# Optimization experiments

Hardware: AMD Instinct MI355X
Metric: run time of the kernel (lower is better)

Reference implementation:

```python
import jax, jax.numpy as jnp
import numpy as np

W0 = 30.0  # Sine frequency


def _bilinear_sample(plane, gx, gy):
    """torch.grid_sample(mode='bilinear', padding_mode='zeros', align_corners=True).
    plane: (C,H,W); gx,gy: (P,) normalized coords in [-1,1]. Returns (P,C)."""
    C, H, W = plane.shape
    ix = (gx + 1.0) * 0.5 * (W - 1)
    iy = (gy + 1.0) * 0.5 * (H - 1)
    x0 = jnp.floor(ix); y0 = jnp.floor(iy)
    x1 = x0 + 1.0;      y1 = y0 + 1.0
    wx1 = ix - x0; wx0 = 1.0 - wx1
    wy1 = iy - y0; wy0 = 1.0 - wy1

    def corner(xc, yc, w):
        valid = ((xc >= 0) & (xc <= W - 1) & (yc >= 0) & (yc <= H - 1)).astype(plane.dtype)
        xi = jnp.clip(xc, 0, W - 1).astype(jnp.int32)
        yi = jnp.clip(yc, 0, H - 1).astype(jnp.int32)
        return plane[:, yi, xi] * (w * valid)  # (C,P)

    out = (corner(x0, y0, wx0 * wy0) + corner(x1, y0, wx1 * wy0)
           + corner(x0, y1, wx0 * wy1) + corner(x1, y1, wx1 * wy1))
    return out.T  # (P,C)


def setup_inputs() -> dict:
    key = jax.random.key(0)
    ks = jax.random.split(key, 8)
    N = 500_000
    C, H, W = 128, 256, 256
    coords = jax.random.uniform(ks[0], (1, N, 3), jnp.float32, minval=-1.0, maxval=1.0)
    planes = [jax.random.normal(ks[1 + i], (1, C, H, W), jnp.float32) * 0.1 for i in range(3)]
    # Linear weights: first layer sine init, then frequency_init(30) for layers 2,3
    W1 = jax.random.uniform(ks[4], (C, C), jnp.float32, minval=-1.0 / C, maxval=1.0 / C)
    lim = np.sqrt(6.0 / C) / W0
    W2 = jax.random.uniform(ks[5], (C, C), jnp.float32, minval=-lim, maxval=lim)
    W3 = jax.random.uniform(ks[6], (1, C), jnp.float32, minval=-lim, maxval=lim)
    return {
        "coordinates": coords,
        "plane_xy": planes[0], "plane_yz": planes[1], "plane_xz": planes[2],
        "W1": W1, "b1": jnp.zeros((C,), jnp.float32),
        "W2": W2, "b2": jnp.zeros((C,), jnp.float32),
        "W3": W3, "b3": jnp.zeros((1,), jnp.float32),
    }


def reference(coordinates, plane_xy, plane_yz, plane_xz, W1, b1, W2, b2, W3, b3):
    B, N, _ = coordinates.shape  # B must be 1 (plane batch is 1, as in torch)
    c = coordinates.reshape(-1, 3)
    p0 = plane_xy[0]
    # NOTE: original module samples the *xz* coords from embeddings[0] (plane_xy) —
    # a bug we faithfully preserve — and multiplies [xy, xz, xz]; yz_embed is unused.
    xy = _bilinear_sample(p0, c[:, 0], c[:, 1])  # (P,C)
    xz = _bilinear_sample(p0, c[:, 0], c[:, 2])  # (P,C)
    features = xy * xz * xz
    h = jnp.sin(W0 * (features @ W1.T + b1))
    h = jnp.sin(W0 * (h @ W2.T + b2))
    out = h @ W3.T + b3
    return out.reshape(B, N, 1)
```

## Files before the change

### kernel.cpp

```cpp
#include <hip/hip_runtime.h>
#include <hip/hip_fp16.h>

typedef float f32x4 __attribute__((ext_vector_type(4)));
typedef _Float16 f16x8 __attribute__((ext_vector_type(8)));

#define CDIM 128
#define HW 256
#define NBINS 256
#define BINCAP 2560
#define TILES_PER_BIN 10
#define BINS_PER_XCD 32
#define GRID_MAIN 256

#define LDS_FENCE() asm volatile("" ::: "memory")

__global__ __launch_bounds__(256) void k_transpose(const float* __restrict__ plane,
                                                   unsigned short* __restrict__ planeT) {
    __shared__ unsigned short tile[32][130];
    int tid = threadIdx.x;
    int y  = blockIdx.x >> 3;
    int x0 = (blockIdx.x & 7) * 32;
    int tx = tid & 31, tc = tid >> 5;
    for (int cc = 0; cc < 128; cc += 8) {
        int c = cc + tc;
        float v = plane[c * (HW * HW) + y * HW + x0 + tx];
        tile[tx][c] = __half_as_ushort(__float2half(v));
    }
    __syncthreads();
    for (int it = 0; it < 16; ++it) {
        int idx = it * 256 + tid;
        int c = idx & 127, xi = idx >> 7;
        planeT[(y * HW + x0 + xi) * CDIM + c] = tile[xi][c];
    }
}

__global__ __launch_bounds__(256) void k_wconv(const float* __restrict__ W1,
                                               const float* __restrict__ W2,
                                               unsigned short* __restrict__ W1h,
                                               unsigned short* __restrict__ W2h) {
    int i = blockIdx.x * 256 + threadIdx.x;
    if (i < 16384) W1h[i] = __half_as_ushort(__float2half(W1[i]));
    else           W2h[i - 16384] = __half_as_ushort(__float2half(W2[i - 16384]));
}

__global__ __launch_bounds__(256) void k_scatter(const float* __restrict__ coords,
                                                 float4* __restrict__ bins,
                                                 int* __restrict__ cursor, int N) {
    __shared__ int hist[NBINS];
    __shared__ int rnk[NBINS];
    __shared__ int base[NBINS];
    const int tid = threadIdx.x;
    hist[tid] = 0; rnk[tid] = 0;
    __syncthreads();

    const int start = blockIdx.x * 2048;
    float gx[8], gy[8], gz[8]; int bn[8];
#pragma unroll
    for (int k = 0; k < 8; ++k) {
        int p = start + k * 256 + tid;
        if (p < N) {
            gx[k] = coords[p * 3 + 0];
            gy[k] = coords[p * 3 + 1];
            gz[k] = coords[p * 3 + 2];
            float ix = (gx[k] + 1.f) * 127.5f;
            bn[k] = max(0, min((int)floorf(ix), HW - 1));
            atomicAdd(&hist[bn[k]], 1);
        } else bn[k] = -1;
    }
    __syncthreads();
    if (hist[tid] > 0) base[tid] = atomicAdd(&cursor[tid], hist[tid]);
    __syncthreads();
#pragma unroll
    for (int k = 0; k < 8; ++k) {
        if (bn[k] >= 0) {
            int p = start + k * 256 + tid;
            int r = atomicAdd(&rnk[bn[k]], 1);
            int pos = base[bn[k]] + r;
            if (pos < BINCAP) {
                float4 rec; rec.x = gx[k]; rec.y = gy[k]; rec.z = gz[k];
                rec.w = __int_as_float(p);
                bins[(size_t)bn[k] * BINCAP + pos] = rec;
            }
        }
    }
}

struct PrepT {
    int off[8];
    __half2 w[4];
    __half2 v[4];
};

__device__ __forceinline__ PrepT prepV(float gx, float gy, float gz, int cg) {
    PrepT r;
    float ix = (gx + 1.f) * 127.5f;
    float iy = (gy + 1.f) * 127.5f;
    float iz = (gz + 1.f) * 127.5f;
    float xf = floorf(ix), yf = floorf(iy), zf = floorf(iz);
    float wx1 = ix - xf, wy1 = iy - yf, wz1 = iz - zf;
    float wx0 = 1.f - wx1, wy0 = 1.f - wy1, wz0 = 1.f - wz1;
    int x0 = max(0, min((int)xf, HW - 1));
    int y0 = max(0, min((int)yf, HW - 1));
    int z0 = max(0, min((int)zf, HW - 1));
    int x1 = min(x0 + 1, HW - 1);
    int y1 = min(y0 + 1, HW - 1);
    int z1 = min(z0 + 1, HW - 1);
    int cx0 = x0 * CDIM + cg * 8, cx1 = x1 * CDIM + cg * 8;
    r.off[0] = (y0 << 15) + cx0; r.off[1] = (y0 << 15) + cx1;
    r.off[2] = (y1 << 15) + cx0; r.off[3] = (y1 << 15) + cx1;
    r.off[4] = (z0 << 15) + cx0; r.off[5] = (z0 << 15) + cx1;
    r.off[6] = (z1 << 15) + cx0; r.off[7] = (z1 << 15) + cx1;
    r.w[0] = __float2half2_rn(wy0 * wx0);
    r.w[1] = __float2half2_rn(wy0 * wx1);
    r.w[2] = __float2half2_rn(wy1 * wx0);
    r.w[3] = __float2half2_rn(wy1 * wx1);
    r.v[0] = __float2half2_rn(wz0 * wx0);
    r.v[1] = __float2half2_rn(wz0 * wx1);
    r.v[2] = __float2half2_rn(wz1 * wx0);
    r.v[3] = __float2half2_rn(wz1 * wx1);
    return r;
}

struct LdT { uint4 d[8]; };

__device__ __forceinline__ LdT ld8(const unsigned short* __restrict__ planeT, const PrepT& a) {
    LdT r;
#pragma unroll
    for (int c = 0; c < 8; ++c)
        r.d[c] = *reinterpret_cast<const uint4*>(planeT + a.off[c]);
    return r;
}

__device__ __forceinline__ __half2 geth2(const uint4& u, int g) {
    const unsigned* p = reinterpret_cast<const unsigned*>(&u);
    return __builtin_bit_cast(__half2, p[g]);
}

__device__ __forceinline__ void interp_store(unsigned short* dst, const PrepT& a, const LdT& L) {
    unsigned o[4];
#pragma unroll
    for (int g = 0; g < 4; ++g) {
        __half2 xy = __hmul2(a.w[0], geth2(L.d[0], g));
        xy = __hfma2(a.w[1], geth2(L.d[1], g), xy);
        xy = __hfma2(a.w[2], geth2(L.d[2], g), xy);
        xy = __hfma2(a.w[3], geth2(L.d[3], g), xy);
        __half2 xz = __hmul2(a.v[0], geth2(L.d[4], g));
        xz = __hfma2(a.v[1], geth2(L.d[5], g), xz);
        xz = __hfma2(a.v[2], geth2(L.d[6], g), xz);
        xz = __hfma2(a.v[3], geth2(L.d[7], g), xz);
        __half2 f = __hmul2(xy, __hmul2(xz, xz));
        o[g] = __builtin_bit_cast(unsigned, f);
    }
    uint4 pack; pack.x = o[0]; pack.y = o[1]; pack.z = o[2]; pack.w = o[3];
    *reinterpret_cast<uint4*>(dst) = pack;
}

template <bool SORTED>
__global__ __launch_bounds__(1024, 4) void k_all(const float* __restrict__ coords,
                                                 const float4* __restrict__ bins,
                                                 const int* __restrict__ cursor,
                                                 const unsigned short* __restrict__ planeT,
                                                 const unsigned short* __restrict__ W1h,
                                                 const unsigned short* __restrict__ W2h,
                                                 const float* __restrict__ b1,
                                                 const float* __restrict__ b2,
                                                 const float* __restrict__ W3,
                                                 const float* __restrict__ b3,
                                                 float* __restrict__ out, int N) {
    __shared__ alignas(16) uint4 W1L[128][16];
    __shared__ alignas(16) uint4 W2L[128][16];
    __shared__ alignas(16) unsigned short featS[256][128];

    const int tid  = threadIdx.x;
    const int wave = tid >> 6, lane = tid & 63;
    const int ro   = wave * 16;
    const int j = lane & 15, rg = lane >> 4;
    const int pt = lane >> 4, cg = lane & 15;

#pragma unroll
    for (int i = 0; i < 2; ++i) {
        int idx = i * 1024 + tid;
        int row = idx >> 4, col = idx & 15;
        W1L[row][col ^ (row & 15)] = reinterpret_cast<const uint4*>(W1h)[idx];
        W2L[row][col ^ (row & 15)] = reinterpret_cast<const uint4*>(W2h)[idx];
    }
    float b1v[8], b2v[8], w3v[8];
#pragma unroll
    for (int nt = 0; nt < 8; ++nt) {
        b1v[nt] = 30.f * b1[nt * 16 + j];
        b2v[nt] = 30.f * b2[nt * 16 + j];
        w3v[nt] = W3[nt * 16 + j];
    }
    const float bb3 = b3[0];
    __syncthreads();

    const int ntt = SORTED ? (NBINS * TILES_PER_BIN) : ((N + 255) >> 8);
    for (int tt = blockIdx.x; tt < ntt; tt += gridDim.x) {
        int bin = 0, base = 0, cnt = 0, pbase = 0;
        if (SORTED) {
            int xcd = tt & 7, jj = tt >> 3;
            bin  = xcd * BINS_PER_XCD + jj / TILES_PER_BIN;
            base = (jj % TILES_PER_BIN) * 256;
            cnt  = min(cursor[bin], BINCAP);
            if (base >= cnt) continue;
        } else {
            pbase = tt * 256 + ro;
        }
        const float4* brec = bins + (size_t)bin * BINCAP;

        {
            PrepT a0, a1, a2, a3;
#pragma unroll
            for (int it = 0; it < 4; ++it) {
                float gx, gy, gz;
                if (SORTED) {
                    int q = min(base + ro + it * 4 + pt, cnt - 1);
                    float4 s = brec[q];
                    gx = s.x; gy = s.y; gz = s.z;
                } else {
                    int p = min(pbase + it * 4 + pt, N - 1);
                    gx = coords[p * 3 + 0];
                    gy = coords[p * 3 + 1];
                    gz = coords[p * 3 + 2];
                }
                PrepT a = prepV(gx, gy, gz, cg);
                if (it == 0) a0 = a; else if (it == 1) a1 = a;
                else if (it == 2) a2 = a; else a3 = a;
            }
            LdT d0 = ld8(planeT, a0);
            LdT d1 = ld8(planeT, a1);
            LdT d2 = ld8(planeT, a2);
            LdT d3 = ld8(planeT, a3);
            interp_store(&featS[ro + 0 * 4 + pt][(cg ^ (0 * 4 + pt)) * 8], a0, d0);
            interp_store(&featS[ro + 1 * 4 + pt][(cg ^ (1 * 4 + pt)) * 8], a1, d1);
            interp_store(&featS[ro + 2 * 4 + pt][(cg ^ (2 * 4 + pt)) * 8], a2, d2);
            interp_store(&featS[ro + 3 * 4 + pt][(cg ^ (3 * 4 + pt)) * 8], a3, d3);
        }

        LDS_FENCE();

        f32x4 acc[8];
#pragma unroll
        for (int nt = 0; nt < 8; ++nt) acc[nt] = (f32x4){0.f, 0.f, 0.f, 0.f};

        f16x8 af[4];
#pragma unroll
        for (int kk = 0; kk < 4; ++kk)
            af[kk] = __builtin_bit_cast(f16x8, *reinterpret_cast<const uint4*>(&featS[ro + j][((kk * 4 + rg) ^ j) * 8]));

#pragma unroll
        for (int kk = 0; kk < 4; ++kk) {
            f16x8 bf[8];
#pragma unroll
            for (int nt = 0; nt < 8; ++nt)
                bf[nt] = __builtin_bit_cast(f16x8, W1L[nt * 16 + j][(kk * 4 + rg) ^ j]);
#pragma unroll
            for (int nt = 0; nt < 8; ++nt)
                acc[nt] = __builtin_amdgcn_mfma_f32_16x16x32_f16(af[kk], bf[nt], acc[nt], 0, 0, 0);
        }

        LDS_FENCE();

#pragma unroll
        for (int nt = 0; nt < 8; ++nt) {
#pragma unroll
            for (int r = 0; r < 4; ++r) {
                float h = __sinf(fmaf(30.f, acc[nt][r], b1v[nt]));
                int row = rg * 4 + r;
                int g = (nt * 2 + (j >> 3)) ^ row;
                featS[ro + row][g * 8 + (j & 7)] = __half_as_ushort(__float2half(h));
            }
        }

        LDS_FENCE();

        f32x4 acc2[8];
#pragma unroll
        for (int nt = 0; nt < 8; ++nt) acc2[nt] = (f32x4){0.f, 0.f, 0.f, 0.f};

        f16x8 af2[4];
#pragma unroll
        for (int kk = 0; kk < 4; ++kk)
            af2[kk] = __builtin_bit_cast(f16x8, *reinterpret_cast<const uint4*>(&featS[ro + j][((kk * 4 + rg) ^ j) * 8]));

#pragma unroll
        for (int kk = 0; kk < 4; ++kk) {
            f16x8 bf[8];
#pragma unroll
            for (int nt = 0; nt < 8; ++nt)
                bf[nt] = __builtin_bit_cast(f16x8, W2L[nt * 16 + j][(kk * 4 + rg) ^ j]);
#pragma unroll
            for (int nt = 0; nt < 8; ++nt)
                acc2[nt] = __builtin_amdgcn_mfma_f32_16x16x32_f16(af2[kk], bf[nt], acc2[nt], 0, 0, 0);
        }

        float part[4] = {0.f, 0.f, 0.f, 0.f};
#pragma unroll
        for (int nt = 0; nt < 8; ++nt) {
#pragma unroll
            for (int r = 0; r < 4; ++r)
                part[r] += __sinf(fmaf(30.f, acc2[nt][r], b2v[nt])) * w3v[nt];
        }
#pragma unroll
        for (int off = 1; off < 16; off <<= 1) {
#pragma unroll
            for (int r = 0; r < 4; ++r) part[r] += __shfl_xor(part[r], off, 64);
        }
        if (j == 0) {
#pragma unroll
            for (int r = 0; r < 4; ++r) {
                int pl = rg * 4 + r;
                if (SORTED) {
                    if (base + ro + pl < cnt) {
                        int orig = __float_as_int(brec[base + ro + pl].w);
                        out[orig] = part[r] + bb3;
                    }
                } else {
                    int p = pbase + pl;
                    if (p < N) out[p] = part[r] + bb3;
                }
            }
        }

        LDS_FENCE();
    }
}

extern "C" void kernel_launch(void* const* d_in, const int* in_sizes, int n_in,
                              void* d_out, int out_size, void* d_ws, size_t ws_size,
                              hipStream_t stream) {
    const float* coords = (const float*)d_in[0];
    const float* plane  = (const float*)d_in[1];
    const float* W1     = (const float*)d_in[4];
    const float* b1     = (const float*)d_in[5];
    const float* W2     = (const float*)d_in[6];
    const float* b2     = (const float*)d_in[7];
    const float* W3     = (const float*)d_in[8];
    const float* b3     = (const float*)d_in[9];
    float* out = (float*)d_out;
    int N = in_sizes[0] / 3;

    char* ws = (char*)d_ws;
    unsigned short* planeT = (unsigned short*)ws;
    unsigned short* W1h = (unsigned short*)(ws + 16777216);
    unsigned short* W2h = (unsigned short*)(ws + 16809984);
    int*    cursor = (int*)(ws + 16842752);
    float4* bins   = (float4*)(ws + 16843776);
    const size_t need = 16843776 + (size_t)NBINS * BINCAP * 16;

    k_transpose<<<dim3(HW * 8), dim3(256), 0, stream>>>(plane, planeT);
    k_wconv<<<dim3(128), dim3(256), 0, stream>>>(W1, W2, W1h, W2h);

    if (ws_size >= need) {
        hipMemsetAsync(cursor, 0, NBINS * sizeof(int), stream);
        k_scatter<<<dim3((N + 2047) / 2048), dim3(256), 0, stream>>>(coords, bins, cursor, N);
        k_all<true><<<dim3(GRID_MAIN), dim3(1024), 0, stream>>>(
            coords, bins, cursor, planeT, W1h, W2h, b1, b2, W3, b3, out, N);
    } else {
        k_all<false><<<dim3(GRID_MAIN), dim3(1024), 0, stream>>>(
            coords, bins, cursor, planeT, W1h, W2h, b1, b2, W3, b3, out, N);
    }
}
```

Measured before the change: 119.0 us.

## Switch MLP to 32x32x16 MFMA with 32-row wave tiles and 640-thread blocks

Each wave now handles 32 points instead of 16 and uses 32x32x16 f16 MFMA in place of 16x16x32, which halves the B-fragment LDS reads per point and changes the accumulator layout and the sine write-back swizzle. Blocks shrink to 10 waves with 320-point tiles and 8 tiles per bin, so a 2560-capacity bin still maps onto whole tiles. The gather loop no longer batches four loads before interpolating, which may reduce memory-level parallelism. The final reduction now needs a 5-step shuffle over 16 registers.

```diff
diff --git a/kernel.cpp b/kernel.cpp
--- a/kernel.cpp
+++ b/kernel.cpp
@@ -1,14 +1,15 @@
 #include <hip/hip_runtime.h>
 #include <hip/hip_fp16.h>
 
-typedef float f32x4 __attribute__((ext_vector_type(4)));
+typedef float f32x16 __attribute__((ext_vector_type(16)));
 typedef _Float16 f16x8 __attribute__((ext_vector_type(8)));
 
 #define CDIM 128
 #define HW 256
 #define NBINS 256
 #define BINCAP 2560
-#define TILES_PER_BIN 10
+#define PTILE 320
+#define TILES_PER_BIN 8
 #define BINS_PER_XCD 32
 #define GRID_MAIN 256
 
@@ -156,168 +157,160 @@
 }
 
 template <bool SORTED>
-__global__ __launch_bounds__(1024, 4) void k_all(const float* __restrict__ coords,
-                                                 const float4* __restrict__ bins,
-                                                 const int* __restrict__ cursor,
-                                                 const unsigned short* __restrict__ planeT,
-                                                 const unsigned short* __restrict__ W1h,
-                                                 const unsigned short* __restrict__ W2h,
-                                                 const float* __restrict__ b1,
-                                                 const float* __restrict__ b2,
-                                                 const float* __restrict__ W3,
-                                                 const float* __restrict__ b3,
-                                                 float* __restrict__ out, int N) {
+__global__ __launch_bounds__(640, 2) void k_all(const float* __restrict__ coords,
+                                                const float4* __restrict__ bins,
+                                                const int* __restrict__ cursor,
+                                                const unsigned short* __restrict__ planeT,
+                                                const unsigned short* __restrict__ W1h,
+                                                const unsigned short* __restrict__ W2h,
+                                                const float* __restrict__ b1,
+                                                const float* __restrict__ b2,
+                                                const float* __restrict__ W3,
+                                                const float* __restrict__ b3,
+                                                float* __restrict__ out, int N) {
     __shared__ alignas(16) uint4 W1L[128][16];
     __shared__ alignas(16) uint4 W2L[128][16];
-    __shared__ alignas(16) unsigned short featS[256][128];
+    __shared__ alignas(16) unsigned short featS[PTILE][128];
 
     const int tid  = threadIdx.x;
     const int wave = tid >> 6, lane = tid & 63;
-    const int ro   = wave * 16;
-    const int j = lane & 15, rg = lane >> 4;
-    const int pt = lane >> 4, cg = lane & 15;
-
-#pragma unroll
-    for (int i = 0; i < 2; ++i) {
-        int idx = i * 1024 + tid;
+    const int ro2  = wave * 32;
+    const int l31 = lane & 31, hi = lane >> 5;
+    const int pt = (lane >> 4) & 3, cg = lane & 15;
+
+    for (int idx = tid; idx < 4096; idx += 640) {
         int row = idx >> 4, col = idx & 15;
         W1L[row][col ^ (row & 15)] = reinterpret_cast<const uint4*>(W1h)[idx];
         W2L[row][col ^ (row & 15)] = reinterpret_cast<const uint4*>(W2h)[idx];
     }
-    float b1v[8], b2v[8], w3v[8];
-#pragma unroll
-    for (int nt = 0; nt < 8; ++nt) {
-        b1v[nt] = 30.f * b1[nt * 16 + j];
-        b2v[nt] = 30.f * b2[nt * 16 + j];
-        w3v[nt] = W3[nt * 16 + j];
+    float b1v[4], b2v[4], w3v[4];
+#pragma unroll
+    for (int nt = 0; nt < 4; ++nt) {
+        b1v[nt] = 30.f * b1[nt * 32 + l31];
+        b2v[nt] = 30.f * b2[nt * 32 + l31];
+        w3v[nt] = W3[nt * 32 + l31];
     }
     const float bb3 = b3[0];
     __syncthreads();
 
-    const int ntt = SORTED ? (NBINS * TILES_PER_BIN) : ((N + 255) >> 8);
+    const int ntt = SORTED ? (NBINS * TILES_PER_BIN) : ((N + PTILE - 1) / PTILE);
     for (int tt = blockIdx.x; tt < ntt; tt += gridDim.x) {
         int bin = 0, base = 0, cnt = 0, pbase = 0;
         if (SORTED) {
             int xcd = tt & 7, jj = tt >> 3;
             bin  = xcd * BINS_PER_XCD + jj / TILES_PER_BIN;
-            base = (jj % TILES_PER_BIN) * 256;
+            base = (jj % TILES_PER_BIN) * PTILE;
             cnt  = min(cursor[bin], BINCAP);
             if (base >= cnt) continue;
         } else {
-            pbase = tt * 256 + ro;
+            pbase = tt * PTILE + ro2;
         }
         const float4* brec = bins + (size_t)bin * BINCAP;
 
-        {
-            PrepT a0, a1, a2, a3;
-#pragma unroll
-            for (int it = 0; it < 4; ++it) {
-                float gx, gy, gz;
+#pragma unroll
+        for (int it = 0; it < 8; ++it) {
+            int pl = it * 4 + pt;
+            float gx, gy, gz;
+            if (SORTED) {
+                int q = min(base + ro2 + pl, cnt - 1);
+                float4 s = brec[q];
+                gx = s.x; gy = s.y; gz = s.z;
+            } else {
+                int p = min(pbase + pl, N - 1);
+                gx = coords[p * 3 + 0];
+                gy = coords[p * 3 + 1];
+                gz = coords[p * 3 + 2];
+            }
+            PrepT a = prepV(gx, gy, gz, cg);
+            LdT   d = ld8(planeT, a);
+            interp_store(&featS[ro2 + pl][(cg ^ (pl & 15)) * 8], a, d);
+        }
+
+        LDS_FENCE();
+
+        f32x16 acc[4];
+#pragma unroll
+        for (int nt = 0; nt < 4; ++nt)
+            acc[nt] = (f32x16){0,0,0,0,0,0,0,0,0,0,0,0,0,0,0,0};
+
+#pragma unroll
+        for (int kk = 0; kk < 8; ++kk) {
+            f16x8 af = __builtin_bit_cast(f16x8, *reinterpret_cast<const uint4*>(
+                &featS[ro2 + l31][((kk * 2 + hi) ^ (lane & 15)) * 8]));
+            f16x8 bf[4];
+#pragma unroll
+            for (int nt = 0; nt < 4; ++nt) {
+                int wrow = nt * 32 + l31;
+                bf[nt] = __builtin_bit_cast(f16x8, W1L[wrow][(kk * 2 + hi) ^ (wrow & 15)]);
+            }
+#pragma unroll
+            for (int nt = 0; nt < 4; ++nt)
+                acc[nt] = __builtin_amdgcn_mfma_f32_32x32x16_f16(af, bf[nt], acc[nt], 0, 0, 0);
+        }
+
+        LDS_FENCE();
+
+#pragma unroll
+        for (int nt = 0; nt < 4; ++nt) {
+#pragma unroll
+            for (int reg = 0; reg < 16; ++reg) {
+                float h = __sinf(fmaf(30.f, acc[nt][reg], b1v[nt]));
+                int row = (reg & 3) + 8 * (reg >> 2) + 4 * hi;
+                int g = (nt * 4 + (l31 >> 3)) ^ (row & 15);
+                featS[ro2 + row][g * 8 + (lane & 7)] = __half_as_ushort(__float2half(h));
+            }
+        }
+
+        LDS_FENCE();
+
+        f32x16 acc2[4];
+#pragma unroll
+        for (int nt = 0; nt < 4; ++nt)
+            acc2[nt] = (f32x16){0,0,0,0,0,0,0,0,0,0,0,0,0,0,0,0};
+
+#pragma unroll
+        for (int kk = 0; kk < 8; ++kk) {
+            f16x8 af2 = __builtin_bit_cast(f16x8, *reinterpret_cast<const uint4*>(
+                &featS[ro2 + l31][((kk * 2 + hi) ^ (lane & 15)) * 8]));
+            f16x8 bf[4];
+#pragma unroll
+            for (int nt = 0; nt < 4; ++nt) {
+                int wrow = nt * 32 + l31;
+                bf[nt] = __builtin_bit_cast(f16x8, W2L[wrow][(kk * 2 + hi) ^ (wrow & 15)]);
+            }
+#pragma unroll
+            for (int nt = 0; nt < 4; ++nt)
+                acc2[nt] = __builtin_amdgcn_mfma_f32_32x32x16_f16(af2, bf[nt], acc2[nt], 0, 0, 0);
+        }
+
+        float part[16];
+#pragma unroll
+        for (int reg = 0; reg < 16; ++reg) {
+            float s = 0.f;
+#pragma unroll
+            for (int nt = 0; nt < 4; ++nt)
+                s += __sinf(fmaf(30.f, acc2[nt][reg], b2v[nt])) * w3v[nt];
+            part[reg] = s;
+        }
+#pragma unroll
+        for (int off = 1; off < 32; off <<= 1) {
+#pragma unroll
+            for (int reg = 0; reg < 16; ++reg)
+                part[reg] += __shfl_xor(part[reg], off, 64);
+        }
+        if (l31 == 0) {
+#pragma unroll
+            for (int reg = 0; reg < 16; ++reg) {
+                int row = (reg & 3) + 8 * (reg >> 2) + 4 * hi;
                 if (SORTED) {
-                    int q = min(base + ro + it * 4 + pt, cnt - 1);
-                    float4 s = brec[q];
-                    gx = s.x; gy = s.y; gz = s.z;
-                } else {
-                    int p = min(pbase + it * 4 + pt, N - 1);
-                    gx = coords[p * 3 + 0];
-                    gy = coords[p * 3 + 1];
-                    gz = coords[p * 3 + 2];
-                }
-                PrepT a = prepV(gx, gy, gz, cg);
-                if (it == 0) a0 = a; else if (it == 1) a1 = a;
-                else if (it == 2) a2 = a; else a3 = a;
-            }
-            LdT d0 = ld8(planeT, a0);
-            LdT d1 = ld8(planeT, a1);
-            LdT d2 = ld8(planeT, a2);
-            LdT d3 = ld8(planeT, a3);
-            interp_store(&featS[ro + 0 * 4 + pt][(cg ^ (0 * 4 + pt)) * 8], a0, d0);
-            interp_store(&featS[ro + 1 * 4 + pt][(cg ^ (1 * 4 + pt)) * 8], a1, d1);
-            interp_store(&featS[ro + 2 * 4 + pt][(cg ^ (2 * 4 + pt)) * 8], a2, d2);
-            interp_store(&featS[ro + 3 * 4 + pt][(cg ^ (3 * 4 + pt)) * 8], a3, d3);
-        }
-
-        LDS_FENCE();
-
-        f32x4 acc[8];
-#pragma unroll
-        for (int nt = 0; nt < 8; ++nt) acc[nt] = (f32x4){0.f, 0.f, 0.f, 0.f};
-
-        f16x8 af[4];
-#pragma unroll
-        for (int kk = 0; kk < 4; ++kk)
-            af[kk] = __builtin_bit_cast(f16x8, *reinterpret_cast<const uint4*>(&featS[ro + j][((kk * 4 + rg) ^ j) * 8]));
-
-#pragma unroll
-        for (int kk = 0; kk < 4; ++kk) {
-            f16x8 bf[8];
-#pragma unroll
-            for (int nt = 0; nt < 8; ++nt)
-                bf[nt] = __builtin_bit_cast(f16x8, W1L[nt * 16 + j][(kk * 4 + rg) ^ j]);
-#pragma unroll
-            for (int nt = 0; nt < 8; ++nt)
-                acc[nt] = __builtin_amdgcn_mfma_f32_16x16x32_f16(af[kk], bf[nt], acc[nt], 0, 0, 0);
-        }
-
-        LDS_FENCE();
-
-#pragma unroll
-        for (int nt = 0; nt < 8; ++nt) {
-#pragma unroll
-            for (int r = 0; r < 4; ++r) {
-                float h = __sinf(fmaf(30.f, acc[nt][r], b1v[nt]));
-                int row = rg * 4 + r;
-                int g = (nt * 2 + (j >> 3)) ^ row;
-                featS[ro + row][g * 8 + (j & 7)] = __half_as_ushort(__float2half(h));
-            }
-        }
-
-        LDS_FENCE();
-
-        f32x4 acc2[8];
-#pragma unroll
-        for (int nt = 0; nt < 8; ++nt) acc2[nt] = (f32x4){0.f, 0.f, 0.f, 0.f};
-
-        f16x8 af2[4];
-#pragma unroll
-        for (int kk = 0; kk < 4; ++kk)
-            af2[kk] = __builtin_bit_cast(f16x8, *reinterpret_cast<const uint4*>(&featS[ro + j][((kk * 4 + rg) ^ j) * 8]));
-
-#pragma unroll
-        for (int kk = 0; kk < 4; ++kk) {
-            f16x8 bf[8];
-#pragma unroll
-            for (int nt = 0; nt < 8; ++nt)
-                bf[nt] = __builtin_bit_cast(f16x8, W2L[nt * 16 + j][(kk * 4 + rg) ^ j]);
-#pragma unroll
-            for (int nt = 0; nt < 8; ++nt)
-                acc2[nt] = __builtin_amdgcn_mfma_f32_16x16x32_f16(af2[kk], bf[nt], acc2[nt], 0, 0, 0);
-        }
-
-        float part[4] = {0.f, 0.f, 0.f, 0.f};
-#pragma unroll
-        for (int nt = 0; nt < 8; ++nt) {
-#pragma unroll
-            for (int r = 0; r < 4; ++r)
-                part[r] += __sinf(fmaf(30.f, acc2[nt][r], b2v[nt])) * w3v[nt];
-        }
-#pragma unroll
-        for (int off = 1; off < 16; off <<= 1) {
-#pragma unroll
-            for (int r = 0; r < 4; ++r) part[r] += __shfl_xor(part[r], off, 64);
-        }
-        if (j == 0) {
-#pragma unroll
-            for (int r = 0; r < 4; ++r) {
-                int pl = rg * 4 + r;
-                if (SORTED) {
-                    if (base + ro + pl < cnt) {
-                        int orig = __float_as_int(brec[base + ro + pl].w);
-                        out[orig] = part[r] + bb3;
+                    int q = base + ro2 + row;
+                    if (q < cnt) {
+                        int orig = __float_as_int(brec[q].w);
+                        out[orig] = part[reg] + bb3;
                     }
                 } else {
-                    int p = pbase + pl;
-                    if (p < N) out[p] = part[r] + bb3;
+                    int p = pbase + row;
+                    if (p < N) out[p] = part[reg] + bb3;
                 }
             }
         }
@@ -354,10 +347,10 @@
     if (ws_size >= need) {
         hipMemsetAsync(cursor, 0, NBINS * sizeof(int), stream);
         k_scatter<<<dim3((N + 2047) / 2048), dim3(256), 0, stream>>>(coords, bins, cursor, N);
-        k_all<true><<<dim3(GRID_MAIN), dim3(1024), 0, stream>>>(
+        k_all<true><<<dim3(GRID_MAIN), dim3(640), 0, stream>>>(
             coords, bins, cursor, planeT, W1h, W2h, b1, b2, W3, b3, out, N);
     } else {
-        k_all<false><<<dim3(GRID_MAIN), dim3(1024), 0, stream>>>(
+        k_all<false><<<dim3(GRID_MAIN), dim3(640), 0, stream>>>(
             coords, bins, cursor, planeT, W1h, W2h, b1, b2, W3, b3, out, N);
     }
 }
```

Measured after the change: 143.5 us. 1.21x slower.
